# Performance work log

Hardware: AMD Instinct MI355X
Metric: run time of the kernel (lower is better)

Reference implementation:

```python
import jax, jax.numpy as jnp
import numpy as np

B, N, E = 4, 10000, 160000
NODE_DIM, EDGE_DIM, HIDDEN, HEADS = 128, 64, 256, 8
HEAD_DIM = HIDDEN // HEADS
LN_EPS = 1e-5


def setup_inputs() -> dict:
    key = jax.random.key(0)
    ks = jax.random.split(key, 11)
    s = 0.05  # stand-in for xavier scale
    return {
        "node_feat": jax.random.normal(ks[0], (B, N, NODE_DIM), dtype=jnp.float32),
        "edge_index": jax.random.randint(ks[1], (2, E), 0, N, dtype=jnp.int64),
        "edge_attr": jax.random.normal(ks[2], (B, E, EDGE_DIM), dtype=jnp.float32),
        "W_node": jax.random.normal(ks[3], (NODE_DIM, HIDDEN), dtype=jnp.float32) * s,
        "W_edge": jax.random.normal(ks[4], (EDGE_DIM, HIDDEN), dtype=jnp.float32) * s,
        "W_res": jax.random.normal(ks[5], (NODE_DIM, HIDDEN), dtype=jnp.float32) * s,
        "att_src": jax.random.normal(ks[6], (HEADS, HEAD_DIM), dtype=jnp.float32) * s,
        "att_dst": jax.random.normal(ks[7], (HEADS, HEAD_DIM), dtype=jnp.float32) * s,
        "att_edge": jax.random.normal(ks[8], (HEADS, HEAD_DIM), dtype=jnp.float32) * s,
        "ln_gamma": jnp.ones((HIDDEN,), dtype=jnp.float32),
        "ln_beta": jnp.zeros((HIDDEN,), dtype=jnp.float32),
    }


def reference(node_feat, edge_index, edge_attr, W_node, W_edge, W_res,
              att_src, att_dst, att_edge, ln_gamma, ln_beta):
    b, n, _ = node_feat.shape
    e_cnt = edge_attr.shape[1]
    src = edge_index[0]
    dst = edge_index[1]

    h = (node_feat @ W_node).reshape(b, n, HEADS, HEAD_DIM)          # [B,N,H,D]
    e = (edge_attr @ W_edge).reshape(b, e_cnt, HEADS, HEAD_DIM)       # [B,E,H,D]
    h_src = h[:, src]                                                 # [B,E,H,D]
    h_dst = h[:, dst]                                                 # [B,E,H,D]

    logits = (jnp.einsum('behd,hd->beh', h_src, att_src)
              + jnp.einsum('behd,hd->beh', h_dst, att_dst)
              + jnp.einsum('behd,hd->beh', e, att_edge))              # [B,E,H]
    logits = jax.nn.leaky_relu(logits, negative_slope=0.2)

    # segment softmax over edges grouped by dst node (edge-leading layout)
    lt = logits.transpose(1, 0, 2)                                    # [E,B,H]
    seg_max = jax.ops.segment_max(lt, dst, num_segments=n)            # [N,B,H]
    ex = jnp.exp(lt - seg_max[dst])
    seg_sum = jax.ops.segment_sum(ex, dst, num_segments=n)            # [N,B,H]
    alpha = ex / seg_sum[dst]                                         # [E,B,H]

    msg = alpha[..., None] * (h_src + e).transpose(1, 0, 2, 3)        # [E,B,H,D]
    agg = jax.ops.segment_sum(msg, dst, num_segments=n)               # [N,B,H,D]
    out = agg.transpose(1, 0, 2, 3).reshape(b, n, HIDDEN)             # [B,N,HIDDEN]

    x = out + node_feat @ W_res
    mu = jnp.mean(x, axis=-1, keepdims=True)
    var = jnp.mean(jnp.square(x - mu), axis=-1, keepdims=True)
    x = (x - mu) * jax.lax.rsqrt(var + LN_EPS) * ln_gamma + ln_beta
    return jax.nn.elu(x)
```

## Files before the change

### kernel.cpp

```cpp
#include <hip/hip_runtime.h>

#define BB 4
#define NN 10000
#define EE 160000
#define HID 256
#define NHEAD 8

typedef __attribute__((ext_vector_type(8))) short short8v;
typedef __attribute__((ext_vector_type(4))) float f32x4;

__device__ __forceinline__ unsigned short f2bf(float f) {
  unsigned u = __float_as_uint(f);
  unsigned r = (u + 0x7fffu + ((u >> 16) & 1u)) >> 16;
  return (unsigned short)r;
}
__device__ __forceinline__ float bf2f(unsigned short u) {
  return __uint_as_float(((unsigned)u) << 16);
}

__global__ void k_prep(const float* __restrict__ We, const float* __restrict__ ae,
                       float* __restrict__ What, unsigned short* __restrict__ We16) {
  int t = threadIdx.x;
  int k = t >> 3, hh = t & 7;
  float s = 0.f;
#pragma unroll
  for (int d = 0; d < 32; ++d) s += We[k * HID + hh * 32 + d] * ae[hh * 32 + d];
  What[k * NHEAD + hh] = s;
  for (int j = t; j < 64 * HID; j += 512) We16[j] = f2bf(We[j]);
}

__global__ __launch_bounds__(256) void k_pack(const float* __restrict__ Wn,
                                              const float* __restrict__ Wr,
                                              unsigned short* __restrict__ Bpack) {
  const int nt = blockIdx.x;
  const int ks = threadIdx.x >> 6;
  const int l = threadIdx.x & 63;
  const int col = nt * 16 + (l & 15);
  const int k0 = ks * 32 + (l >> 4) * 8;
  const float* __restrict__ src = (nt < 16) ? Wn : Wr;
  const int c2 = col & 255;
  short8v v;
#pragma unroll
  for (int e = 0; e < 8; ++e) v[e] = f2bf(src[(k0 + e) * HID + c2]);
  *reinterpret_cast<short8v*>(Bpack + ((size_t)(nt * 4 + ks) * 64 + l) * 8) = v;
}

__global__ __launch_bounds__(512) void k_projm(
    const float* __restrict__ nf,
    const unsigned short* __restrict__ Bpack,
    unsigned short* __restrict__ h16, float* __restrict__ out) {
  const int t = threadIdx.x;
  const int w = t >> 6, l = t & 63;
  const int base = blockIdx.x * 64 + (w & 3) * 16;
  const int nhalf = w >> 2;
  const int arow = base + (l & 15);
  short8v a[4];
#pragma unroll
  for (int ks = 0; ks < 4; ++ks) {
    const float* p = nf + (size_t)arow * 128 + ks * 32 + (l >> 4) * 8;
    const float4 f0 = *reinterpret_cast<const float4*>(p);
    const float4 f1 = *reinterpret_cast<const float4*>(p + 4);
    short8v v;
    v[0] = f2bf(f0.x); v[1] = f2bf(f0.y); v[2] = f2bf(f0.z); v[3] = f2bf(f0.w);
    v[4] = f2bf(f1.x); v[5] = f2bf(f1.y); v[6] = f2bf(f1.z); v[7] = f2bf(f1.w);
    a[ks] = v;
  }
  f32x4 acc[16];
#pragma unroll
  for (int i = 0; i < 16; ++i) acc[i] = (f32x4){0.f, 0.f, 0.f, 0.f};
  const short8v* bp =
      reinterpret_cast<const short8v*>(Bpack) + (size_t)nhalf * 4096 + l;
#pragma unroll
  for (int nt = 0; nt < 16; ++nt) {
#pragma unroll
    for (int ks = 0; ks < 4; ++ks) {
      const short8v bf = bp[(nt * 4 + ks) * 64];
      acc[nt] = __builtin_amdgcn_mfma_f32_16x16x32_bf16(a[ks], bf, acc[nt], 0, 0, 0);
    }
  }
  unsigned short* __restrict__ resOv = reinterpret_cast<unsigned short*>(out);
#pragma unroll
  for (int b = 0; b < 4; ++b) {
    const int bn = base + (l >> 4) * 4 + b;
    if (nhalf == 0) {
      const int bb = bn / NN, n = bn - bb * NN;
      unsigned short* __restrict__ rowp = h16 + (((size_t)n * 4 + bb) << 8);
#pragma unroll
      for (int nt = 0; nt < 16; ++nt) rowp[nt * 16 + (l & 15)] = f2bf(acc[nt][b]);
    } else {
      unsigned short* __restrict__ rowp = resOv + ((size_t)bn << 9);
#pragma unroll
      for (int nt = 0; nt < 16; ++nt) rowp[nt * 16 + (l & 15)] = f2bf(acc[nt][b]);
    }
  }
}

__global__ __launch_bounds__(256) void k_att(
    const unsigned short* __restrict__ h16, const float* __restrict__ as_,
    const float* __restrict__ ad_, float* __restrict__ ssrc,
    float* __restrict__ sdst) {
  const int w = threadIdx.x >> 6, l = threadIdx.x & 63;
  const size_t bn = (size_t)blockIdx.x * 4 + w;
  const int b = (int)(bn / NN), n = (int)(bn - (size_t)b * NN);
  const ushort4 hv =
      *reinterpret_cast<const ushort4*>(h16 + (((size_t)n * 4 + b) << 8) + 4 * l);
  const float4 av = reinterpret_cast<const float4*>(as_)[l];
  const float4 dv = reinterpret_cast<const float4*>(ad_)[l];
  const float x0 = bf2f(hv.x), x1 = bf2f(hv.y), x2 = bf2f(hv.z), x3 = bf2f(hv.w);
  float ps = x0 * av.x + x1 * av.y + x2 * av.z + x3 * av.w;
  float pd = x0 * dv.x + x1 * dv.y + x2 * dv.z + x3 * dv.w;
#pragma unroll
  for (int off = 1; off <= 4; off <<= 1) {
    ps += __shfl_xor(ps, off);
    pd += __shfl_xor(pd, off);
  }
  if ((l & 7) == 0) {
    ssrc[bn * NHEAD + (l >> 3)] = ps;
    sdst[bn * NHEAD + (l >> 3)] = pd;
  }
}

__global__ void k_hist(const int* __restrict__ ei, int* __restrict__ cnt) {
  int e = blockIdx.x * 256 + threadIdx.x;
  if (e < EE) atomicAdd(&cnt[ei[EE + e]], 1);
}

__global__ __launch_bounds__(1024) void k_scan(const int* __restrict__ cnt,
                                               int* __restrict__ off) {
  __shared__ int ls[1024];
  const int t = threadIdx.x;
  int own = 0;
  int deg[10];
  if (t < 1000) {
#pragma unroll
    for (int i = 0; i < 10; ++i) { deg[i] = cnt[t * 10 + i]; own += deg[i]; }
  }
  ls[t] = own;
  __syncthreads();
  for (int s = 1; s < 1024; s <<= 1) {
    int v = 0;
    if (t >= s) v = ls[t - s];
    __syncthreads();
    if (t >= s) ls[t] += v;
    __syncthreads();
  }
  if (t < 1000) {
    int start = ls[t] - own;
#pragma unroll
    for (int i = 0; i < 10; ++i) { off[t * 10 + i] = start; start += deg[i]; }
  }
  if (t == 0) off[NN] = EE;
}

__global__ void k_scatter(const int* __restrict__ ei, const int* __restrict__ off,
                          int* __restrict__ cur, int2* __restrict__ eidx,
                          int* __restrict__ inv) {
  int e = blockIdx.x * 256 + threadIdx.x;
  if (e >= EE) return;
  int s = ei[e], d = ei[EE + e];
  int pos = off[d] + atomicAdd(&cur[d], 1);
  eidx[pos] = make_int2(e, s);
  inv[e] = pos;
}

__global__ __launch_bounds__(256) void k_elogit(
    const float* __restrict__ ea, const int* __restrict__ ei,
    const float* __restrict__ What, const float* __restrict__ ssrc,
    const float* __restrict__ sdst, const int* __restrict__ inv,
    float* __restrict__ exP) {
  __shared__ float sea[32 * 65];
  __shared__ float sw[64 * NHEAD];
  const int t = threadIdx.x;
  sw[t] = What[t];
  sw[t + 256] = What[t + 256];
  const int g0 = blockIdx.x * 32;
  const float* base = ea + (size_t)g0 * 64;
#pragma unroll
  for (int j = 0; j < 8; ++j) {
    int f = t + j * 256;
    sea[(f >> 6) * 65 + (f & 63)] = base[f];
  }
  __syncthreads();
  const int il = t >> 3, hh = t & 7;
  const int g = g0 + il;
  float acc = 0.f;
#pragma unroll
  for (int k = 0; k < 64; ++k) acc += sea[il * 65 + k] * sw[k * NHEAD + hh];
  const int b = g / EE, e = g - b * EE;
  const int src = ei[e], dst = ei[EE + e];
  float lg = ssrc[((size_t)b * NN + src) * NHEAD + hh] +
             sdst[((size_t)b * NN + dst) * NHEAD + hh] + acc;
  lg = lg > 0.f ? lg : 0.2f * lg;
  const int pos = inv[e];
  exP[(((size_t)pos * 4 + b) << 3) + hh] = __expf(lg);
}

__global__ __launch_bounds__(256) void k_agg(
    const float* __restrict__ ea, const unsigned short* __restrict__ h16,
    const float* __restrict__ exP, const int* __restrict__ off,
    const int2* __restrict__ eidx, const unsigned short* __restrict__ We16,
    const float* __restrict__ gam, const float* __restrict__ bet,
    float* __restrict__ out) {
  __shared__ float zsh[4][8 * 65];
  const int wid = threadIdx.x >> 6, l = threadIdx.x & 63;
  const int b = wid, node = blockIdx.x;
  const int start = off[node], end = off[node + 1];
  const int hq = l >> 3;
  const int hr = l & 7;
  float4 u4 = {0.f, 0.f, 0.f, 0.f};
  float z0 = 0.f, z1 = 0.f, z2 = 0.f, z3 = 0.f;
  float z4 = 0.f, z5 = 0.f, z6 = 0.f, z7 = 0.f;
  float ss = 0.f;
  const float* __restrict__ exb = exP + ((size_t)b << 3);
  const float* __restrict__ eab = ea + (size_t)b * EE * 64;
  const unsigned short* __restrict__ hb = h16 + ((size_t)b << 8);
#pragma unroll 4
  for (int i = start; i < end; ++i) {
    const int2 es = eidx[i];
    const float* exi = exb + ((size_t)i << 5);
    const float4 xa = *reinterpret_cast<const float4*>(exi);
    const float4 xb = *reinterpret_cast<const float4*>(exi + 4);
    const float exu = exi[hq];
    ss += exi[hr];
    const float eal = eab[(size_t)es.x * 64 + l];
    const ushort4 h4 =
        *reinterpret_cast<const ushort4*>(hb + ((size_t)es.y << 10) + 4 * l);
    z0 += xa.x * eal; z1 += xa.y * eal; z2 += xa.z * eal; z3 += xa.w * eal;
    z4 += xb.x * eal; z5 += xb.y * eal; z6 += xb.z * eal; z7 += xb.w * eal;
    u4.x += exu * bf2f(h4.x); u4.y += exu * bf2f(h4.y);
    u4.z += exu * bf2f(h4.z); u4.w += exu * bf2f(h4.w);
  }
  zsh[wid][0 * 65 + l] = z0; zsh[wid][1 * 65 + l] = z1;
  zsh[wid][2 * 65 + l] = z2; zsh[wid][3 * 65 + l] = z3;
  zsh[wid][4 * 65 + l] = z4; zsh[wid][5 * 65 + l] = z5;
  zsh[wid][6 * 65 + l] = z6; zsh[wid][7 * 65 + l] = z7;
  const size_t bn = (size_t)b * NN + node;
  const ushort4 r16 = *reinterpret_cast<const ushort4*>(
      reinterpret_cast<const unsigned short*>(out) + (bn << 9) + 4 * l);
#pragma unroll 8
  for (int k = 0; k < 64; ++k) {
    const float zk = zsh[wid][hq * 65 + k];
    const ushort4 wv = *reinterpret_cast<const ushort4*>(We16 + (k << 8) + 4 * l);
    u4.x += zk * bf2f(wv.x); u4.y += zk * bf2f(wv.y);
    u4.z += zk * bf2f(wv.z); u4.w += zk * bf2f(wv.w);
  }
  const float ssq = __shfl(ss, hq);
  const float sc = ssq > 0.f ? 1.f / ssq : 0.f;
  u4.x = u4.x * sc + bf2f(r16.x); u4.y = u4.y * sc + bf2f(r16.y);
  u4.z = u4.z * sc + bf2f(r16.z); u4.w = u4.w * sc + bf2f(r16.w);
  float s1 = u4.x + u4.y + u4.z + u4.w;
  float s2 = u4.x * u4.x + u4.y * u4.y + u4.z * u4.z + u4.w * u4.w;
#pragma unroll
  for (int off2 = 1; off2 <= 32; off2 <<= 1) {
    s1 += __shfl_xor(s1, off2);
    s2 += __shfl_xor(s2, off2);
  }
  const float mu = s1 * (1.f / HID);
  const float var = s2 * (1.f / HID) - mu * mu;
  const float rstd = rsqrtf(var + 1e-5f);
  const float4 g4 = reinterpret_cast<const float4*>(gam)[l];
  const float4 b4 = reinterpret_cast<const float4*>(bet)[l];
  float4 y;
  y.x = (u4.x - mu) * rstd * g4.x + b4.x;
  y.y = (u4.y - mu) * rstd * g4.y + b4.y;
  y.z = (u4.z - mu) * rstd * g4.z + b4.z;
  y.w = (u4.w - mu) * rstd * g4.w + b4.w;
  y.x = y.x > 0.f ? y.x : expm1f(y.x);
  y.y = y.y > 0.f ? y.y : expm1f(y.y);
  y.z = y.z > 0.f ? y.z : expm1f(y.z);
  y.w = y.w > 0.f ? y.w : expm1f(y.w);
  *reinterpret_cast<float4*>(out + (bn << 8) + 4 * l) = y;
}

extern "C" void kernel_launch(void* const* d_in, const int* in_sizes, int n_in,
                              void* d_out, int out_size, void* d_ws, size_t ws_size,
                              hipStream_t stream) {
  const float* nf   = (const float*)d_in[0];
  const int*   ei   = (const int*)d_in[1];
  const float* eatt = (const float*)d_in[2];
  const float* Wn   = (const float*)d_in[3];
  const float* We   = (const float*)d_in[4];
  const float* Wr   = (const float*)d_in[5];
  const float* as_  = (const float*)d_in[6];
  const float* ad_  = (const float*)d_in[7];
  const float* ae_  = (const float*)d_in[8];
  const float* gam  = (const float*)d_in[9];
  const float* bet  = (const float*)d_in[10];
  float* out = (float*)d_out;

  char* ws = (char*)d_ws;
  size_t o = 0;
  auto alloc = [&](size_t bytes) -> void* {
    void* p = ws + o;
    o += (bytes + 255) & ~(size_t)255;
    return p;
  };
  unsigned short* h16  = (unsigned short*)alloc((size_t)BB * NN * HID * 2);
  float* ssrc   = (float*)alloc((size_t)BB * NN * NHEAD * 4);
  float* sdst   = (float*)alloc((size_t)BB * NN * NHEAD * 4);
  float* What   = (float*)alloc(64 * NHEAD * 4);
  unsigned short* We16 = (unsigned short*)alloc(64 * HID * 2);
  float* exP    = (float*)alloc((size_t)BB * EE * NHEAD * 4);
  int*  cnt     = (int*)alloc(NN * 4);
  int*  cur     = (int*)alloc(NN * 4);
  int*  offn    = (int*)alloc((NN + 1) * 4);
  int2* eidx    = (int2*)alloc((size_t)EE * 8);
  int*  inv     = (int*)alloc((size_t)EE * 4);
  unsigned short* Bpack = (unsigned short*)alloc((size_t)512 * 128 * 2);

  hipLaunchKernelGGL(k_prep, dim3(1), dim3(512), 0, stream, We, ae_, What, We16);
  hipLaunchKernelGGL(k_pack, dim3(32), dim3(256), 0, stream, Wn, Wr, Bpack);
  hipLaunchKernelGGL(k_projm, dim3(BB * NN / 64), dim3(512), 0, stream,
                     nf, Bpack, h16, out);
  hipLaunchKernelGGL(k_att, dim3(BB * NN / 4), dim3(256), 0, stream,
                     h16, as_, ad_, ssrc, sdst);
  hipMemsetAsync(cnt, 0, NN * 4, stream);
  hipMemsetAsync(cur, 0, NN * 4, stream);
  hipLaunchKernelGGL(k_hist, dim3((EE + 255) / 256), dim3(256), 0, stream, ei, cnt);
  hipLaunchKernelGGL(k_scan, dim3(1), dim3(1024), 0, stream, cnt, offn);
  hipLaunchKernelGGL(k_scatter, dim3((EE + 255) / 256), dim3(256), 0, stream,
                     ei, offn, cur, eidx, inv);
  hipLaunchKernelGGL(k_elogit, dim3(BB * EE / 32), dim3(256), 0, stream,
                     eatt, ei, What, ssrc, sdst, inv, exP);
  hipLaunchKernelGGL(k_agg, dim3(NN), dim3(256), 0, stream,
                     eatt, h16, exP, offn, eidx, We16, gam, bet, out);
}
```

Baseline: 284.8 us.

## Split each node's edge loop across two wave halves in aggregation kernel

The aggregation kernel now runs 512 threads per node, so each batch has two waves that each process half of the node's incoming edges. The per-edge z and u partial sums are merged through shared memory, and the 64-wide edge-weight projection is split by k between the two halves. Separately, the two counter memsets are merged into one call. This doubles the parallelism available for the latency-bound gather loop, at the cost of extra shared memory, two block barriers, and idle waves during the LayerNorm epilogue.

```diff
diff --git a/kernel.cpp b/kernel.cpp
--- a/kernel.cpp
+++ b/kernel.cpp
@@ -195,16 +195,22 @@
   exP[(((size_t)pos * 4 + b) << 3) + hh] = __expf(lg);
 }
 
-__global__ __launch_bounds__(256) void k_agg(
+__global__ __launch_bounds__(512) void k_agg(
     const float* __restrict__ ea, const unsigned short* __restrict__ h16,
     const float* __restrict__ exP, const int* __restrict__ off,
     const int2* __restrict__ eidx, const unsigned short* __restrict__ We16,
     const float* __restrict__ gam, const float* __restrict__ bet,
     float* __restrict__ out) {
-  __shared__ float zsh[4][8 * 65];
-  const int wid = threadIdx.x >> 6, l = threadIdx.x & 63;
-  const int b = wid, node = blockIdx.x;
-  const int start = off[node], end = off[node + 1];
+  __shared__ float zsh[8][8 * 65];
+  __shared__ float ush[4][64][4];
+  __shared__ float sssh[4][64];
+  const int w = threadIdx.x >> 6, l = threadIdx.x & 63;
+  const int b = w & 3, half = w >> 2;
+  const int node = blockIdx.x;
+  const int s0 = off[node], e0 = off[node + 1];
+  const int mid = s0 + ((e0 - s0 + 1) >> 1);
+  const int start = half ? mid : s0;
+  const int end = half ? e0 : mid;
   const int hq = l >> 3;
   const int hr = l & 7;
   float4 u4 = {0.f, 0.f, 0.f, 0.f};
@@ -230,20 +236,32 @@
     u4.x += exu * bf2f(h4.x); u4.y += exu * bf2f(h4.y);
     u4.z += exu * bf2f(h4.z); u4.w += exu * bf2f(h4.w);
   }
-  zsh[wid][0 * 65 + l] = z0; zsh[wid][1 * 65 + l] = z1;
-  zsh[wid][2 * 65 + l] = z2; zsh[wid][3 * 65 + l] = z3;
-  zsh[wid][4 * 65 + l] = z4; zsh[wid][5 * 65 + l] = z5;
-  zsh[wid][6 * 65 + l] = z6; zsh[wid][7 * 65 + l] = z7;
+  zsh[w][0 * 65 + l] = z0; zsh[w][1 * 65 + l] = z1;
+  zsh[w][2 * 65 + l] = z2; zsh[w][3 * 65 + l] = z3;
+  zsh[w][4 * 65 + l] = z4; zsh[w][5 * 65 + l] = z5;
+  zsh[w][6 * 65 + l] = z6; zsh[w][7 * 65 + l] = z7;
+  __syncthreads();
+  const int k0 = half << 5;
+#pragma unroll 8
+  for (int k = k0; k < k0 + 32; ++k) {
+    const float zk = zsh[b][hq * 65 + k] + zsh[b + 4][hq * 65 + k];
+    const ushort4 wv = *reinterpret_cast<const ushort4*>(We16 + (k << 8) + 4 * l);
+    u4.x += zk * bf2f(wv.x); u4.y += zk * bf2f(wv.y);
+    u4.z += zk * bf2f(wv.z); u4.w += zk * bf2f(wv.w);
+  }
+  if (half) {
+    ush[b][l][0] = u4.x; ush[b][l][1] = u4.y;
+    ush[b][l][2] = u4.z; ush[b][l][3] = u4.w;
+    sssh[b][l] = ss;
+  }
+  __syncthreads();
+  if (half) return;
+  u4.x += ush[b][l][0]; u4.y += ush[b][l][1];
+  u4.z += ush[b][l][2]; u4.w += ush[b][l][3];
+  ss += sssh[b][l];
   const size_t bn = (size_t)b * NN + node;
   const ushort4 r16 = *reinterpret_cast<const ushort4*>(
       reinterpret_cast<const unsigned short*>(out) + (bn << 9) + 4 * l);
-#pragma unroll 8
-  for (int k = 0; k < 64; ++k) {
-    const float zk = zsh[wid][hq * 65 + k];
-    const ushort4 wv = *reinterpret_cast<const ushort4*>(We16 + (k << 8) + 4 * l);
-    u4.x += zk * bf2f(wv.x); u4.y += zk * bf2f(wv.y);
-    u4.z += zk * bf2f(wv.z); u4.w += zk * bf2f(wv.w);
-  }
   const float ssq = __shfl(ss, hq);
   const float sc = ssq > 0.f ? 1.f / ssq : 0.f;
   u4.x = u4.x * sc + bf2f(r16.x); u4.y = u4.y * sc + bf2f(r16.y);
@@ -301,8 +319,10 @@
   float* What   = (float*)alloc(64 * NHEAD * 4);
   unsigned short* We16 = (unsigned short*)alloc(64 * HID * 2);
   float* exP    = (float*)alloc((size_t)BB * EE * NHEAD * 4);
+  size_t cnt_off = o;
   int*  cnt     = (int*)alloc(NN * 4);
   int*  cur     = (int*)alloc(NN * 4);
+  size_t cnt_bytes = o - cnt_off;
   int*  offn    = (int*)alloc((NN + 1) * 4);
   int2* eidx    = (int2*)alloc((size_t)EE * 8);
   int*  inv     = (int*)alloc((size_t)EE * 4);
@@ -314,14 +334,13 @@
                      nf, Bpack, h16, out);
   hipLaunchKernelGGL(k_att, dim3(BB * NN / 4), dim3(256), 0, stream,
                      h16, as_, ad_, ssrc, sdst);
-  hipMemsetAsync(cnt, 0, NN * 4, stream);
-  hipMemsetAsync(cur, 0, NN * 4, stream);
+  hipMemsetAsync(ws + cnt_off, 0, cnt_bytes, stream);
   hipLaunchKernelGGL(k_hist, dim3((EE + 255) / 256), dim3(256), 0, stream, ei, cnt);
   hipLaunchKernelGGL(k_scan, dim3(1), dim3(1024), 0, stream, cnt, offn);
   hipLaunchKernelGGL(k_scatter, dim3((EE + 255) / 256), dim3(256), 0, stream,
                      ei, offn, cur, eidx, inv);
   hipLaunchKernelGGL(k_elogit, dim3(BB * EE / 32), dim3(256), 0, stream,
                      eatt, ei, What, ssrc, sdst, inv, exP);
-  hipLaunchKernelGGL(k_agg, dim3(NN), dim3(256), 0, stream,
+  hipLaunchKernelGGL(k_agg, dim3(NN), dim3(512), 0, stream,
                      eatt, h16, exP, offn, eidx, We16, gam, bet, out);
 }
```

After: 324.3 us. +13.8%, slower.

## Fuse attention scores into projection and pre-permute bf16 edge features

Applied to the files above, without the earlier changes.

Merges the weight-prep and pack kernels into one launch. Computes the per-head source and destination attention scores in the projection kernel's MFMA epilogue, removing a separate kernel. The edge-logit kernel now also writes edge_attr as bf16 in dst-sorted order, so aggregation reads contiguous half-size data instead of gathering fp32 rows by edge id. This costs an extra intermediate buffer write, and edge features lose precision by going through bf16.

```diff
diff --git a/kernel.cpp b/kernel.cpp
--- a/kernel.cpp
+++ b/kernel.cpp
@@ -18,27 +18,28 @@
   return __uint_as_float(((unsigned)u) << 16);
 }
 
-__global__ void k_prep(const float* __restrict__ We, const float* __restrict__ ae,
-                       float* __restrict__ What, unsigned short* __restrict__ We16) {
-  int t = threadIdx.x;
-  int k = t >> 3, hh = t & 7;
-  float s = 0.f;
-#pragma unroll
-  for (int d = 0; d < 32; ++d) s += We[k * HID + hh * 32 + d] * ae[hh * 32 + d];
-  What[k * NHEAD + hh] = s;
-  for (int j = t; j < 64 * HID; j += 512) We16[j] = f2bf(We[j]);
-}
-
-__global__ __launch_bounds__(256) void k_pack(const float* __restrict__ Wn,
-                                              const float* __restrict__ Wr,
-                                              unsigned short* __restrict__ Bpack) {
+__global__ __launch_bounds__(512) void k_prep(
+    const float* __restrict__ We, const float* __restrict__ ae,
+    const float* __restrict__ Wn, const float* __restrict__ Wr,
+    float* __restrict__ What, unsigned short* __restrict__ We16,
+    unsigned short* __restrict__ Bpack) {
+  const int t = threadIdx.x;
+  if (blockIdx.x == 32) {
+    int k = t >> 3, hh = t & 7;
+    float s = 0.f;
+#pragma unroll
+    for (int d = 0; d < 32; ++d) s += We[k * HID + hh * 32 + d] * ae[hh * 32 + d];
+    What[k * NHEAD + hh] = s;
+    for (int j = t; j < 64 * HID; j += 512) We16[j] = f2bf(We[j]);
+    return;
+  }
+  if (t >= 256) return;
   const int nt = blockIdx.x;
-  const int ks = threadIdx.x >> 6;
-  const int l = threadIdx.x & 63;
-  const int col = nt * 16 + (l & 15);
+  const int ks = t >> 6;
+  const int l = t & 63;
   const int k0 = ks * 32 + (l >> 4) * 8;
   const float* __restrict__ src = (nt < 16) ? Wn : Wr;
-  const int c2 = col & 255;
+  const int c2 = (nt * 16 + (l & 15)) & 255;
   short8v v;
 #pragma unroll
   for (int e = 0; e < 8; ++e) v[e] = f2bf(src[(k0 + e) * HID + c2]);
@@ -46,9 +47,10 @@
 }
 
 __global__ __launch_bounds__(512) void k_projm(
-    const float* __restrict__ nf,
-    const unsigned short* __restrict__ Bpack,
-    unsigned short* __restrict__ h16, float* __restrict__ out) {
+    const float* __restrict__ nf, const unsigned short* __restrict__ Bpack,
+    const float* __restrict__ as_, const float* __restrict__ ad_,
+    unsigned short* __restrict__ h16, float* __restrict__ out,
+    float* __restrict__ ssrc, float* __restrict__ sdst) {
   const int t = threadIdx.x;
   const int w = t >> 6, l = t & 63;
   const int base = blockIdx.x * 64 + (w & 3) * 16;
@@ -93,30 +95,28 @@
       for (int nt = 0; nt < 16; ++nt) rowp[nt * 16 + (l & 15)] = f2bf(acc[nt][b]);
     }
   }
-}
-
-__global__ __launch_bounds__(256) void k_att(
-    const unsigned short* __restrict__ h16, const float* __restrict__ as_,
-    const float* __restrict__ ad_, float* __restrict__ ssrc,
-    float* __restrict__ sdst) {
-  const int w = threadIdx.x >> 6, l = threadIdx.x & 63;
-  const size_t bn = (size_t)blockIdx.x * 4 + w;
-  const int b = (int)(bn / NN), n = (int)(bn - (size_t)b * NN);
-  const ushort4 hv =
-      *reinterpret_cast<const ushort4*>(h16 + (((size_t)n * 4 + b) << 8) + 4 * l);
-  const float4 av = reinterpret_cast<const float4*>(as_)[l];
-  const float4 dv = reinterpret_cast<const float4*>(ad_)[l];
-  const float x0 = bf2f(hv.x), x1 = bf2f(hv.y), x2 = bf2f(hv.z), x3 = bf2f(hv.w);
-  float ps = x0 * av.x + x1 * av.y + x2 * av.z + x3 * av.w;
-  float pd = x0 * dv.x + x1 * dv.y + x2 * dv.z + x3 * dv.w;
-#pragma unroll
-  for (int off = 1; off <= 4; off <<= 1) {
-    ps += __shfl_xor(ps, off);
-    pd += __shfl_xor(pd, off);
-  }
-  if ((l & 7) == 0) {
-    ssrc[bn * NHEAD + (l >> 3)] = ps;
-    sdst[bn * NHEAD + (l >> 3)] = pd;
+  if (nhalf == 0) {
+    const int lo = l & 15;
+#pragma unroll
+    for (int h = 0; h < 8; ++h) {
+      const float a0 = as_[h * 32 + lo], a1 = as_[h * 32 + 16 + lo];
+      const float d0 = ad_[h * 32 + lo], d1 = ad_[h * 32 + 16 + lo];
+#pragma unroll
+      for (int rb = 0; rb < 4; ++rb) {
+        float ps = acc[2 * h][rb] * a0 + acc[2 * h + 1][rb] * a1;
+        float pd = acc[2 * h][rb] * d0 + acc[2 * h + 1][rb] * d1;
+#pragma unroll
+        for (int off = 1; off <= 8; off <<= 1) {
+          ps += __shfl_xor(ps, off);
+          pd += __shfl_xor(pd, off);
+        }
+        if (lo == 0) {
+          const int bn = base + (l >> 4) * 4 + rb;
+          ssrc[(size_t)bn * NHEAD + h] = ps;
+          sdst[(size_t)bn * NHEAD + h] = pd;
+        }
+      }
+    }
   }
 }
 
@@ -153,13 +153,13 @@
 }
 
 __global__ void k_scatter(const int* __restrict__ ei, const int* __restrict__ off,
-                          int* __restrict__ cur, int2* __restrict__ eidx,
+                          int* __restrict__ cur, int* __restrict__ esrc,
                           int* __restrict__ inv) {
   int e = blockIdx.x * 256 + threadIdx.x;
   if (e >= EE) return;
   int s = ei[e], d = ei[EE + e];
   int pos = off[d] + atomicAdd(&cur[d], 1);
-  eidx[pos] = make_int2(e, s);
+  esrc[pos] = s;
   inv[e] = pos;
 }
 
@@ -167,7 +167,7 @@
     const float* __restrict__ ea, const int* __restrict__ ei,
     const float* __restrict__ What, const float* __restrict__ ssrc,
     const float* __restrict__ sdst, const int* __restrict__ inv,
-    float* __restrict__ exP) {
+    float* __restrict__ exP, unsigned short* __restrict__ ea16P) {
   __shared__ float sea[32 * 65];
   __shared__ float sw[64 * NHEAD];
   const int t = threadIdx.x;
@@ -193,14 +193,18 @@
   lg = lg > 0.f ? lg : 0.2f * lg;
   const int pos = inv[e];
   exP[(((size_t)pos * 4 + b) << 3) + hh] = __expf(lg);
+  short8v v8;
+#pragma unroll
+  for (int j = 0; j < 8; ++j) v8[j] = f2bf(sea[il * 65 + hh * 8 + j]);
+  *reinterpret_cast<short8v*>(ea16P + (((size_t)pos * 4 + b) << 6) + hh * 8) = v8;
 }
 
 __global__ __launch_bounds__(256) void k_agg(
-    const float* __restrict__ ea, const unsigned short* __restrict__ h16,
-    const float* __restrict__ exP, const int* __restrict__ off,
-    const int2* __restrict__ eidx, const unsigned short* __restrict__ We16,
-    const float* __restrict__ gam, const float* __restrict__ bet,
-    float* __restrict__ out) {
+    const unsigned short* __restrict__ ea16P,
+    const unsigned short* __restrict__ h16, const float* __restrict__ exP,
+    const int* __restrict__ off, const int* __restrict__ esrc,
+    const unsigned short* __restrict__ We16, const float* __restrict__ gam,
+    const float* __restrict__ bet, float* __restrict__ out) {
   __shared__ float zsh[4][8 * 65];
   const int wid = threadIdx.x >> 6, l = threadIdx.x & 63;
   const int b = wid, node = blockIdx.x;
@@ -212,19 +216,19 @@
   float z4 = 0.f, z5 = 0.f, z6 = 0.f, z7 = 0.f;
   float ss = 0.f;
   const float* __restrict__ exb = exP + ((size_t)b << 3);
-  const float* __restrict__ eab = ea + (size_t)b * EE * 64;
+  const unsigned short* __restrict__ eab16 = ea16P + ((size_t)b << 6);
   const unsigned short* __restrict__ hb = h16 + ((size_t)b << 8);
 #pragma unroll 4
   for (int i = start; i < end; ++i) {
-    const int2 es = eidx[i];
+    const int src = esrc[i];
     const float* exi = exb + ((size_t)i << 5);
     const float4 xa = *reinterpret_cast<const float4*>(exi);
     const float4 xb = *reinterpret_cast<const float4*>(exi + 4);
     const float exu = exi[hq];
     ss += exi[hr];
-    const float eal = eab[(size_t)es.x * 64 + l];
+    const float eal = bf2f(eab16[((size_t)i << 8) + l]);
     const ushort4 h4 =
-        *reinterpret_cast<const ushort4*>(hb + ((size_t)es.y << 10) + 4 * l);
+        *reinterpret_cast<const ushort4*>(hb + ((size_t)src << 10) + 4 * l);
     z0 += xa.x * eal; z1 += xa.y * eal; z2 += xa.z * eal; z3 += xa.w * eal;
     z4 += xb.x * eal; z5 += xb.y * eal; z6 += xb.z * eal; z7 += xb.w * eal;
     u4.x += exu * bf2f(h4.x); u4.y += exu * bf2f(h4.y);
@@ -301,27 +305,27 @@
   float* What   = (float*)alloc(64 * NHEAD * 4);
   unsigned short* We16 = (unsigned short*)alloc(64 * HID * 2);
   float* exP    = (float*)alloc((size_t)BB * EE * NHEAD * 4);
+  size_t cnt_off = o;
   int*  cnt     = (int*)alloc(NN * 4);
   int*  cur     = (int*)alloc(NN * 4);
+  size_t cnt_bytes = o - cnt_off;
   int*  offn    = (int*)alloc((NN + 1) * 4);
-  int2* eidx    = (int2*)alloc((size_t)EE * 8);
+  int*  esrc    = (int*)alloc((size_t)EE * 4);
   int*  inv     = (int*)alloc((size_t)EE * 4);
   unsigned short* Bpack = (unsigned short*)alloc((size_t)512 * 128 * 2);
-
-  hipLaunchKernelGGL(k_prep, dim3(1), dim3(512), 0, stream, We, ae_, What, We16);
-  hipLaunchKernelGGL(k_pack, dim3(32), dim3(256), 0, stream, Wn, Wr, Bpack);
+  unsigned short* ea16P = (unsigned short*)alloc((size_t)EE * BB * 64 * 2);
+
+  hipLaunchKernelGGL(k_prep, dim3(33), dim3(512), 0, stream,
+                     We, ae_, Wn, Wr, What, We16, Bpack);
   hipLaunchKernelGGL(k_projm, dim3(BB * NN / 64), dim3(512), 0, stream,
-                     nf, Bpack, h16, out);
-  hipLaunchKernelGGL(k_att, dim3(BB * NN / 4), dim3(256), 0, stream,
-                     h16, as_, ad_, ssrc, sdst);
-  hipMemsetAsync(cnt, 0, NN * 4, stream);
-  hipMemsetAsync(cur, 0, NN * 4, stream);
+                     nf, Bpack, as_, ad_, h16, out, ssrc, sdst);
+  hipMemsetAsync(ws + cnt_off, 0, cnt_bytes, stream);
   hipLaunchKernelGGL(k_hist, dim3((EE + 255) / 256), dim3(256), 0, stream, ei, cnt);
   hipLaunchKernelGGL(k_scan, dim3(1), dim3(1024), 0, stream, cnt, offn);
   hipLaunchKernelGGL(k_scatter, dim3((EE + 255) / 256), dim3(256), 0, stream,
-                     ei, offn, cur, eidx, inv);
+                     ei, offn, cur, esrc, inv);
   hipLaunchKernelGGL(k_elogit, dim3(BB * EE / 32), dim3(256), 0, stream,
-                     eatt, ei, What, ssrc, sdst, inv, exP);
+                     eatt, ei, What, ssrc, sdst, inv, exP, ea16P);
   hipLaunchKernelGGL(k_agg, dim3(NN), dim3(256), 0, stream,
-                     eatt, h16, exP, offn, eidx, We16, gam, bet, out);
-}
+                     ea16P, h16, exP, offn, esrc, We16, gam, bet, out);
+}
```

Result: slower. 295.9 us (+3.9%).
